# Kernel optimization log

Measured on AMD Instinct MI355X. Metric: run time of the kernel, lower is better.

The kernel has to match this reference:

```python
import jax, jax.numpy as jnp
import numpy as np

B, C, H, W = 2, 128, 64, 64


def setup_inputs() -> dict:
    key = jax.random.key(0)
    ks = jax.random.split(key, 16)
    s = 1.0 / np.sqrt(C)
    d = {
        "x": jax.random.normal(ks[0], (B, C, H, W), jnp.float32),
        "y": jax.random.normal(ks[1], (B, C, H, W), jnp.float32),
    }
    names = ["qr", "qi", "kr", "ki", "vr", "vi"]
    for i, n in enumerate(names):
        d["W" + n] = jax.random.normal(ks[2 + 2 * i], (C, C), jnp.float32) * s
        d["b" + n] = jax.random.normal(ks[3 + 2 * i], (C,), jnp.float32) * s
    return d


def _lin(t, Wt, bt):
    # t: [b, n, c]; torch Linear: t @ W^T + b
    return jnp.einsum("bnc,dc->bnd", t, Wt) + bt


def reference(x, y, Wqr, bqr, Wqi, bqi, Wkr, bkr, Wki, bki, Wvr, bvr, Wvi, bvi):
    b, c, h, w = x.shape
    xf = jnp.fft.fft2(x)  # over last two axes (h, w)
    yf = jnp.fft.fft2(y)
    # b c h w -> b (h w) c
    def flat(t):
        return t.transpose(0, 2, 3, 1).reshape(b, h * w, c)
    xr, xi = flat(xf.real), flat(xf.imag)
    yr, yi = flat(yf.real), flat(yf.imag)

    Qr = _lin(xr, Wqr, bqr) - _lin(xi, Wqi, bqi)
    Qi = _lin(xi, Wqr, bqr) + _lin(xr, Wqi, bqi)
    Kr = _lin(yr, Wkr, bkr) - _lin(yi, Wki, bki)
    Ki = _lin(yi, Wkr, bkr) + _lin(yr, Wki, bki)
    Vr = _lin(yr, Wvr, bvr) - _lin(yi, Wvi, bvi)
    Vi = _lin(yi, Wvr, bvr) + _lin(yr, Wvi, bvi)

    sr = jnp.einsum("bnc,bmc->bnm", Qr, Kr) - jnp.einsum("bnc,bmc->bnm", Qi, Ki)
    si = jnp.einsum("bnc,bmc->bnm", Qr, Ki) + jnp.einsum("bnc,bmc->bnm", Qi, Kr)
    scores = jnp.sqrt(sr * sr + si * si + 1e-8)
    attn = jax.nn.softmax(scores, axis=-1)

    out_r = jnp.einsum("bnm,bmc->bnc", attn, Vr)
    out_i = jnp.einsum("bnm,bmc->bnc", attn, Vi)
    out_c = jax.lax.complex(out_r, out_i)
    # b (h w) c -> b c h w
    out_c = out_c.reshape(b, h, w, c).transpose(0, 3, 1, 2)
    return jnp.fft.ifft2(out_c).real
```

## Files before the change

kernel.cpp:

```cpp
#include <hip/hip_runtime.h>
#include <math.h>


#define PI2 6.283185307179586f

typedef __attribute__((ext_vector_type(8))) short short8;
typedef __attribute__((ext_vector_type(4))) float f32x4;

#define MFMA16(A,B,C) __builtin_amdgcn_mfma_f32_16x16x32_bf16((A),(B),(C),0,0,0)

__device__ inline unsigned short f2bf(float x){
  union{float f; unsigned int u;} a; a.f = x;
  unsigned int r = (a.u + 0x7fffu + ((a.u>>16)&1u)) >> 16;
  return (unsigned short)r;
}
__device__ inline float bf2f(unsigned short h){
  union{unsigned int u; float f;} a; a.u = ((unsigned int)h)<<16; return a.f;
}
__device__ inline short8 neg8(short8 x){
  union{short8 v; unsigned int u[4];} a; a.v = x;
  a.u[0]^=0x80008000u; a.u[1]^=0x80008000u; a.u[2]^=0x80008000u; a.u[3]^=0x80008000u;
  return a.v;
}
__device__ inline void gload_lds16(const void* g, void* lds){
  __builtin_amdgcn_global_load_lds((const __attribute__((address_space(1))) unsigned int*)g,
                                   (__attribute__((address_space(3))) unsigned int*)lds,
                                   16, 0, 0);
}

__global__ __launch_bounds__(256) void dft2_fwd_kernel(
    const float* __restrict__ x, const float* __restrict__ y,
    float* __restrict__ xr, float* __restrict__ xi,
    float* __restrict__ yr, float* __restrict__ yi)
{
  __shared__ float Xs[4096];
  __shared__ float Tr[4096], Ti[4096];
  __shared__ float twc[64], tws[64];
  int blk = blockIdx.x;
  const float* src; float *outr, *outi;
  int plane;
  if (blk < 256) { src = x; outr = xr; outi = xi; plane = blk; }
  else           { src = y; outr = yr; outi = yi; plane = blk - 256; }
  int b = plane >> 7, c = plane & 127;
  int t = threadIdx.x;
  if (t < 64) {
    float ang = -PI2 * (float)t / 64.0f;
    twc[t] = cosf(ang); tws[t] = sinf(ang);
  }
  const float* p = src + ((size_t)plane << 12);
  for (int i = t; i < 4096; i += 256) Xs[i] = p[i];
  __syncthreads();
  for (int j = 0; j < 16; j++) {
    int o = t + 256 * j; int h = o >> 6, wp = o & 63;
    float ar = 0.f, ai = 0.f;
    for (int w = 0; w < 64; w++) {
      int k = (w * wp) & 63;
      float v = Xs[h * 64 + w];
      ar = fmaf(v, twc[k], ar);
      ai = fmaf(v, tws[k], ai);
    }
    Tr[h * 64 + wp] = ar; Ti[h * 64 + wp] = ai;
  }
  __syncthreads();
  size_t ob = ((size_t)b * 4096) * 128 + c;
  for (int j = 0; j < 16; j++) {
    int o = t + 256 * j; int hp = o >> 6, wp = o & 63;
    float ar = 0.f, ai = 0.f;
    for (int h = 0; h < 64; h++) {
      int k = (h * hp) & 63;
      float cr = twc[k], ci = tws[k];
      float tr = Tr[h * 64 + wp], ti = Ti[h * 64 + wp];
      ar += tr * cr - ti * ci;
      ai += tr * ci + ti * cr;
    }
    int n = (hp << 6) + wp;
    outr[ob + (size_t)n * 128] = ar;
    outi[ob + (size_t)n * 128] = ai;
  }
}

__global__ __launch_bounds__(256) void proj_pack_kernel(
    const float* __restrict__ xr, const float* __restrict__ xi,
    const float* __restrict__ yr, const float* __restrict__ yi,
    const float* __restrict__ Wqr, const float* __restrict__ bqr,
    const float* __restrict__ Wqi, const float* __restrict__ bqi,
    const float* __restrict__ Wkr, const float* __restrict__ bkr,
    const float* __restrict__ Wki, const float* __restrict__ bki,
    const float* __restrict__ Wvr, const float* __restrict__ bvr,
    const float* __restrict__ Wvi, const float* __restrict__ bvi,
    unsigned short* __restrict__ Qpk, unsigned short* __restrict__ Kpk,
    unsigned short* __restrict__ Vpk)
{
  __shared__ __align__(16) char smem[65536];
  float* Asr = (float*)smem;
  float* Asi = Asr + 64 * 33;
  float* Wsr = Asi + 64 * 33;
  float* Wsi = Wsr + 128 * 33;
  unsigned short* pk = (unsigned short*)smem;

  int nt = blockIdx.x, lin = blockIdx.y, b = blockIdx.z;
  const float *ar, *ai, *Wr, *Wi, *br_, *bi_;
  if (lin == 0)      { ar = xr; ai = xi; Wr = Wqr; Wi = Wqi; br_ = bqr; bi_ = bqi; }
  else if (lin == 1) { ar = yr; ai = yi; Wr = Wkr; Wi = Wki; br_ = bkr; bi_ = bki; }
  else               { ar = yr; ai = yi; Wr = Wvr; Wi = Wvi; br_ = bvr; bi_ = bvi; }
  int t = threadIdx.x; int td = t & 15, tn = t >> 4;
  int n0 = nt * 64;
  size_t abase = (size_t)b * 4096 * 128 + (size_t)n0 * 128;
  float accr[4][8] = {}, acci[4][8] = {};
  for (int kk = 0; kk < 4; kk++) {
    __syncthreads();
    for (int idx = t; idx < 64 * 32; idx += 256) {
      int r = idx >> 5, ccol = idx & 31;
      Asr[r * 33 + ccol] = ar[abase + (size_t)r * 128 + kk * 32 + ccol];
      Asi[r * 33 + ccol] = ai[abase + (size_t)r * 128 + kk * 32 + ccol];
    }
    for (int idx = t; idx < 128 * 32; idx += 256) {
      int r = idx >> 5, ccol = idx & 31;
      Wsr[r * 33 + ccol] = Wr[(size_t)r * 128 + kk * 32 + ccol];
      Wsi[r * 33 + ccol] = Wi[(size_t)r * 128 + kk * 32 + ccol];
    }
    __syncthreads();
    for (int k = 0; k < 32; k++) {
      float a_r[4], a_i[4], w_r[8], w_i[8];
      #pragma unroll
      for (int i = 0; i < 4; i++) {
        a_r[i] = Asr[(tn * 4 + i) * 33 + k];
        a_i[i] = Asi[(tn * 4 + i) * 33 + k];
      }
      #pragma unroll
      for (int jj = 0; jj < 8; jj++) {
        w_r[jj] = Wsr[(td + 16 * jj) * 33 + k];
        w_i[jj] = Wsi[(td + 16 * jj) * 33 + k];
      }
      #pragma unroll
      for (int i = 0; i < 4; i++)
        #pragma unroll
        for (int jj = 0; jj < 8; jj++) {
          accr[i][jj] += a_r[i] * w_r[jj] - a_i[i] * w_i[jj];
          acci[i][jj] += a_i[i] * w_r[jj] + a_r[i] * w_i[jj];
        }
    }
  }
  __syncthreads();
  for (int jj = 0; jj < 8; jj++) {
    int d = td + 16 * jj;
    float brd = br_[d], bid = bi_[d];
    #pragma unroll
    for (int i = 0; i < 4; i++) {
      int n = n0 + tn * 4 + i;
      float cr = accr[i][jj] + (brd - bid);
      float ci = acci[i][jj] + (brd + bid);
      if (lin <= 1) {
        unsigned short rh = f2bf(cr); unsigned short rl = f2bf(cr - bf2f(rh));
        unsigned short ih = f2bf(ci); unsigned short il = f2bf(ci - bf2f(ih));
        int s = d >> 5, j = d & 7;
        int lq = ((d & 31) >> 3) * 16 + (n & 15);
        int gi = (n >> 4) & 3;
        if (lin == 0) {
          pk[(((gi * 4 + 0) * 4 + s) * 512) + lq * 8 + j] = rh;
          pk[(((gi * 4 + 1) * 4 + s) * 512) + lq * 8 + j] = rl;
          pk[(((gi * 4 + 2) * 4 + s) * 512) + lq * 8 + j] = ih;
          pk[(((gi * 4 + 3) * 4 + s) * 512) + lq * 8 + j] = il;
        } else {
          pk[(((0 * 4 + gi) * 4 + s) * 512) + lq * 8 + j] = rh;
          pk[(((1 * 4 + gi) * 4 + s) * 512) + lq * 8 + j] = rl;
          pk[(((2 * 4 + gi) * 4 + s) * 512) + lq * 8 + j] = ih;
          pk[(((3 * 4 + gi) * 4 + s) * 512) + lq * 8 + j] = il;
        }
      } else {
        int smi = (n >> 5) & 1, jv = n & 7;
        int lv = ((n & 31) >> 3) * 16 + (d & 15);
        pk[(smi * 16 + (d >> 4)) * 512 + lv * 8 + jv] = f2bf(cr);
        pk[(smi * 16 + 8 + (d >> 4)) * 512 + lv * 8 + jv] = f2bf(ci);
      }
    }
  }
  __syncthreads();
  if (lin == 0) {
    int tq0 = nt * 4;
    #pragma unroll
    for (int ch = 0; ch < 16; ch++) {
      int idx = t + 256 * ch;
      int l = idx & 63; int rest = idx >> 6;
      int s = rest & 3, a = (rest >> 2) & 3, gi = rest >> 4;
      short8 v = *(const short8*)(pk + (size_t)idx * 8);
      size_t gaddr = ((size_t)((b * 256 + tq0 + gi) * 16 + a * 4 + s)) * 512 + (size_t)l * 8;
      *(short8*)(Qpk + gaddr) = v;
    }
  } else if (lin == 1) {
    int mt2 = n0 >> 6;
    size_t gbase = ((size_t)(b * 64 + mt2)) * 32768;
    #pragma unroll
    for (int ch = 0; ch < 16; ch++) {
      int idx = t + 256 * ch;
      short8 v = *(const short8*)(pk + (size_t)idx * 8);
      *(short8*)(Kpk + gbase + (size_t)idx * 8) = v;
    }
  } else {
    int sm0 = n0 >> 5;
    size_t gbase = ((size_t)(b * 128 + sm0)) * 8192;
    #pragma unroll
    for (int ch = 0; ch < 8; ch++) {
      int idx = t + 256 * ch;
      short8 v = *(const short8*)(pk + (size_t)idx * 8);
      *(short8*)(Vpk + gbase + (size_t)idx * 8) = v;
    }
  }
}

__global__ __launch_bounds__(512, 1) void attn_mfma_kernel(
    const short* __restrict__ Qpk, const short* __restrict__ Kpk,
    const short* __restrict__ Vpk,
    float* __restrict__ Or_, float* __restrict__ Oi_)
{
  __shared__ __align__(16) short Klds[2][32768];
  __shared__ __align__(16) short Pfrag[4 * 512];
  __shared__ float rmax[2][16][4];
  __shared__ float rsum[2][16][4];

  const int bi = blockIdx.x;
  const int xg = bi & 7;
  const int b = xg >> 2;
  const int qt = (bi >> 3) * 4 + (xg & 3);
  const int t = threadIdx.x;
  const int w = t >> 6, l = t & 63;
  const int qg = w & 1, mh = w >> 1;
  const int g = l >> 4, c = l & 15;

  const short8* Qp8 = (const short8*)Qpk;
  const int tq = qt * 2 + qg;
  short8 Qf[4][4];
  #pragma unroll
  for (int a = 0; a < 4; a++)
    #pragma unroll
    for (int s = 0; s < 4; s++)
      Qf[a][s] = Qp8[((size_t)((b * 256 + tq) * 16 + a * 4 + s)) * 64 + l];

  f32x4 O[4], M, L;
  #pragma unroll
  for (int nt = 0; nt < 4; nt++) O[nt] = (f32x4){0.f, 0.f, 0.f, 0.f};
  M = (f32x4){-3e38f, -3e38f, -3e38f, -3e38f};
  L = (f32x4){0.f, 0.f, 0.f, 0.f};

  const char* Kg = (const char*)Kpk;
  {
    const char* gsrc = Kg + ((size_t)(b * 64) << 16);
    char* lb = (char*)&Klds[0][0];
    #pragma unroll
    for (int i2 = 0; i2 < 8; i2++) {
      int ch = i2 * 8 + w;
      gload_lds16(gsrc + ch * 1024 + l * 16, lb + ch * 1024);
    }
  }
  const short8* Vp8 = (const short8*)Vpk;

  for (int mt = 0; mt < 64; mt++) {
    const int cur = mt & 1;
    __syncthreads();
    if (mt + 1 < 64) {
      const char* gsrc = Kg + ((size_t)(b * 64 + mt + 1) << 16);
      char* lb = (char*)&Klds[cur ^ 1][0];
      #pragma unroll
      for (int i2 = 0; i2 < 8; i2++) {
        int ch = i2 * 8 + w;
        gload_lds16(gsrc + ch * 1024 + l * 16, lb + ch * 1024);
      }
    }
    const short8* kb8 = (const short8*)&Klds[cur][0];
    f32x4 sr = (f32x4){0,0,0,0}, si = (f32x4){0,0,0,0};
    #pragma unroll
    for (int s = 0; s < 4; s++) {
      short8 Brh = kb8[((0 * 4 + mh) * 4 + s) * 64 + l];
      short8 Brl = kb8[((1 * 4 + mh) * 4 + s) * 64 + l];
      short8 Bih = kb8[((2 * 4 + mh) * 4 + s) * 64 + l];
      short8 Bil = kb8[((3 * 4 + mh) * 4 + s) * 64 + l];
      short8 nBih = neg8(Bih), nBil = neg8(Bil);
      sr = MFMA16(Qf[0][s], Brh, sr);
      si = MFMA16(Qf[0][s], Bih, si);
      sr = MFMA16(Qf[1][s], Brh, sr);
      si = MFMA16(Qf[1][s], Bih, si);
      sr = MFMA16(Qf[0][s], Brl, sr);
      si = MFMA16(Qf[0][s], Bil, si);
      sr = MFMA16(Qf[2][s], nBih, sr);
      si = MFMA16(Qf[2][s], Brh, si);
      sr = MFMA16(Qf[3][s], nBih, sr);
      si = MFMA16(Qf[3][s], Brh, si);
      sr = MFMA16(Qf[2][s], nBil, sr);
      si = MFMA16(Qf[2][s], Brl, si);
    }
    f32x4 s0, mx;
    #pragma unroll
    for (int r = 0; r < 4; r++) {
      s0[r] = sqrtf(sr[r] * sr[r] + si[r] * si[r] + 1e-8f);
      mx[r] = s0[r];
    }
    #pragma unroll
    for (int d = 1; d < 16; d <<= 1) {
      #pragma unroll
      for (int r = 0; r < 4; r++) mx[r] = fmaxf(mx[r], __shfl_xor(mx[r], d));
    }
    if (c < 4) rmax[qg][4 * g + c][mh] = mx[c];
    __syncthreads();
    f32x4 nm, esc, p, ps;
    #pragma unroll
    for (int r = 0; r < 4; r++) {
      float v = fmaxf(fmaxf(rmax[qg][4 * g + r][0], rmax[qg][4 * g + r][1]),
                      fmaxf(rmax[qg][4 * g + r][2], rmax[qg][4 * g + r][3]));
      nm[r] = fmaxf(M[r], v);
      esc[r] = __expf(M[r] - nm[r]);
      M[r] = nm[r];
      p[r] = __expf(s0[r] - nm[r]);
      ps[r] = p[r];
    }
    #pragma unroll
    for (int d = 1; d < 16; d <<= 1) {
      #pragma unroll
      for (int r = 0; r < 4; r++) ps[r] += __shfl_xor(ps[r], d);
    }
    if (c < 4) rsum[qg][4 * g + c][mh] = ps[c];
    {
      int ks = mh >> 1;
      int lb2 = ((mh & 1) * 2 + (c >> 3)) * 16;
      int j = c & 7;
      #pragma unroll
      for (int r = 0; r < 4; r++)
        Pfrag[(qg * 2 + ks) * 512 + (lb2 + 4 * g + r) * 8 + j] = (short)f2bf(p[r]);
    }
    __syncthreads();
    #pragma unroll
    for (int r = 0; r < 4; r++) {
      L[r] = L[r] * esc[r] + rsum[qg][4 * g + r][0] + rsum[qg][4 * g + r][1]
                           + rsum[qg][4 * g + r][2] + rsum[qg][4 * g + r][3];
      #pragma unroll
      for (int nt = 0; nt < 4; nt++) O[nt][r] *= esc[r];
    }
    #pragma unroll
    for (int ks = 0; ks < 2; ks++) {
      short8 Pa = *(const short8*)&Pfrag[(qg * 2 + ks) * 512 + l * 8];
      const size_t vb = ((size_t)((b * 128 + mt * 2 + ks) * 16 + mh * 4)) * 64 + l;
      #pragma unroll
      for (int nt = 0; nt < 4; nt++) {
        short8 Vb = Vp8[vb + (size_t)nt * 64];
        O[nt] = MFMA16(Pa, Vb, O[nt]);
      }
    }
  }
  const size_t base = (size_t)b * 4096 * 128;
  f32x4 inv;
  #pragma unroll
  for (int r = 0; r < 4; r++) inv[r] = 1.0f / L[r];
  #pragma unroll
  for (int nt = 0; nt < 4; nt++) {
    int cc = mh * 64 + nt * 16 + c;
    #pragma unroll
    for (int r = 0; r < 4; r++) {
      int row = qt * 32 + qg * 16 + 4 * g + r;
      float v = O[nt][r] * inv[r];
      if (cc < 128) Or_[base + (size_t)row * 128 + cc] = v;
      else          Oi_[base + (size_t)row * 128 + cc - 128] = v;
    }
  }
}

__global__ __launch_bounds__(256) void idft2_kernel(
    const float* __restrict__ Or_, const float* __restrict__ Oi_,
    float* __restrict__ out)
{
  __shared__ float Ar[4096], Ai[4096], Tr[4096], Ti[4096];
  __shared__ float twc[64], tws[64];
  int plane = blockIdx.x; int b = plane >> 7, c = plane & 127;
  int t = threadIdx.x;
  if (t < 64) {
    float ang = PI2 * (float)t / 64.0f;
    twc[t] = cosf(ang); tws[t] = sinf(ang);
  }
  size_t ibase = (size_t)b * 4096 * 128 + c;
  for (int i = t; i < 4096; i += 256) {
    Ar[i] = Or_[ibase + (size_t)i * 128];
    Ai[i] = Oi_[ibase + (size_t)i * 128];
  }
  __syncthreads();
  for (int j = 0; j < 16; j++) {
    int o = t + 256 * j; int hp = o >> 6, w = o & 63;
    float tr = 0.f, ti = 0.f;
    for (int wp = 0; wp < 64; wp++) {
      int k = (wp * w) & 63;
      float cr = twc[k], ci = tws[k];
      float ar = Ar[hp * 64 + wp], ai = Ai[hp * 64 + wp];
      tr += ar * cr - ai * ci;
      ti += ai * cr + ar * ci;
    }
    Tr[hp * 64 + w] = tr; Ti[hp * 64 + w] = ti;
  }
  __syncthreads();
  size_t obase = ((size_t)plane) << 12;
  for (int j = 0; j < 16; j++) {
    int o = t + 256 * j; int h = o >> 6, w = o & 63;
    float acc = 0.f;
    for (int hp = 0; hp < 64; hp++) {
      int k = (hp * h) & 63;
      acc += Tr[hp * 64 + w] * twc[k] - Ti[hp * 64 + w] * tws[k];
    }
    out[obase + o] = acc * (1.0f / 4096.0f);
  }
}

extern "C" void kernel_launch(void* const* d_in, const int* in_sizes, int n_in,
                              void* d_out, int out_size, void* d_ws, size_t ws_size,
                              hipStream_t stream) {
  const float* x   = (const float*)d_in[0];
  const float* y   = (const float*)d_in[1];
  const float* Wqr = (const float*)d_in[2];  const float* bqr = (const float*)d_in[3];
  const float* Wqi = (const float*)d_in[4];  const float* bqi = (const float*)d_in[5];
  const float* Wkr = (const float*)d_in[6];  const float* bkr = (const float*)d_in[7];
  const float* Wki = (const float*)d_in[8];  const float* bki = (const float*)d_in[9];
  const float* Wvr = (const float*)d_in[10]; const float* bvr = (const float*)d_in[11];
  const float* Wvi = (const float*)d_in[12]; const float* bvi = (const float*)d_in[13];
  char* wsb = (char*)d_ws;
  if (ws_size < ((size_t)36 << 20)) return;
  unsigned short* Qpk = (unsigned short*)(wsb);
  unsigned short* Kpk = (unsigned short*)(wsb + ((size_t)8 << 20));
  unsigned short* Vpk = (unsigned short*)(wsb + ((size_t)16 << 20));
  float* xr = (float*)(wsb + ((size_t)20 << 20));
  float* xi = (float*)(wsb + ((size_t)24 << 20));
  float* yr = (float*)(wsb + ((size_t)28 << 20));
  float* yi = (float*)(wsb + ((size_t)32 << 20));
  float* Or_ = (float*)(wsb + ((size_t)20 << 20));
  float* Oi_ = (float*)(wsb + ((size_t)24 << 20));
  float* out = (float*)d_out;

  hipLaunchKernelGGL(dft2_fwd_kernel, dim3(512), dim3(256), 0, stream,
                     x, y, xr, xi, yr, yi);
  hipLaunchKernelGGL(proj_pack_kernel, dim3(64, 3, 2), dim3(256), 0, stream,
                     xr, xi, yr, yi,
                     Wqr, bqr, Wqi, bqi, Wkr, bkr, Wki, bki, Wvr, bvr, Wvi, bvi,
                     Qpk, Kpk, Vpk);
  hipLaunchKernelGGL(attn_mfma_kernel, dim3(256), dim3(512), 0, stream,
                     (const short*)Qpk, (const short*)Kpk, (const short*)Vpk, Or_, Oi_);
  hipLaunchKernelGGL(idft2_kernel, dim3(256), dim3(256), 0, stream,
                     Or_, Oi_, out);
}
```

Baseline: 480.0 us.

## Restructure attention softmax loop to defer PV MFMA and drop a barrier

```diff
diff --git a/kernel.cpp b/kernel.cpp
--- a/kernel.cpp
+++ b/kernel.cpp
@@ -79,66 +79,65 @@
   }
 }
 
-__global__ __launch_bounds__(256) void proj_pack_kernel(
-    const float* __restrict__ xr, const float* __restrict__ xi,
-    const float* __restrict__ yr, const float* __restrict__ yi,
-    const float* __restrict__ Wqr, const float* __restrict__ bqr,
-    const float* __restrict__ Wqi, const float* __restrict__ bqi,
-    const float* __restrict__ Wkr, const float* __restrict__ bkr,
-    const float* __restrict__ Wki, const float* __restrict__ bki,
-    const float* __restrict__ Wvr, const float* __restrict__ bvr,
-    const float* __restrict__ Wvi, const float* __restrict__ bvi,
-    unsigned short* __restrict__ Qpk, unsigned short* __restrict__ Kpk,
-    unsigned short* __restrict__ Vpk)
+template<int LIN>
+__global__ __launch_bounds__(256) void proj_pack_t(
+    const float* __restrict__ ar, const float* __restrict__ ai,
+    const float* __restrict__ Wr, const float* __restrict__ Wi,
+    const float* __restrict__ br_, const float* __restrict__ bi_,
+    unsigned short* __restrict__ outp)
 {
   __shared__ __align__(16) char smem[65536];
   float* Asr = (float*)smem;
-  float* Asi = Asr + 64 * 33;
-  float* Wsr = Asi + 64 * 33;
-  float* Wsi = Wsr + 128 * 33;
+  float* Asi = Asr + 64 * 36;
+  float* Wsr = Asi + 64 * 36;
+  float* Wsi = Wsr + 128 * 36;
   unsigned short* pk = (unsigned short*)smem;
 
-  int nt = blockIdx.x, lin = blockIdx.y, b = blockIdx.z;
-  const float *ar, *ai, *Wr, *Wi, *br_, *bi_;
-  if (lin == 0)      { ar = xr; ai = xi; Wr = Wqr; Wi = Wqi; br_ = bqr; bi_ = bqi; }
-  else if (lin == 1) { ar = yr; ai = yi; Wr = Wkr; Wi = Wki; br_ = bkr; bi_ = bki; }
-  else               { ar = yr; ai = yi; Wr = Wvr; Wi = Wvi; br_ = bvr; bi_ = bvi; }
+  int nt = blockIdx.x, b = blockIdx.y;
   int t = threadIdx.x; int td = t & 15, tn = t >> 4;
   int n0 = nt * 64;
   size_t abase = (size_t)b * 4096 * 128 + (size_t)n0 * 128;
   float accr[4][8] = {}, acci[4][8] = {};
   for (int kk = 0; kk < 4; kk++) {
     __syncthreads();
-    for (int idx = t; idx < 64 * 32; idx += 256) {
-      int r = idx >> 5, ccol = idx & 31;
-      Asr[r * 33 + ccol] = ar[abase + (size_t)r * 128 + kk * 32 + ccol];
-      Asi[r * 33 + ccol] = ai[abase + (size_t)r * 128 + kk * 32 + ccol];
-    }
-    for (int idx = t; idx < 128 * 32; idx += 256) {
-      int r = idx >> 5, ccol = idx & 31;
-      Wsr[r * 33 + ccol] = Wr[(size_t)r * 128 + kk * 32 + ccol];
-      Wsi[r * 33 + ccol] = Wi[(size_t)r * 128 + kk * 32 + ccol];
+    #pragma unroll
+    for (int q2 = 0; q2 < 2; q2++) {
+      int idx = t + 256 * q2; int r = idx >> 3, c4 = (idx & 7) * 4;
+      f32x4 va = *(const f32x4*)&ar[abase + (size_t)r * 128 + kk * 32 + c4];
+      f32x4 vb = *(const f32x4*)&ai[abase + (size_t)r * 128 + kk * 32 + c4];
+      *(f32x4*)&Asr[r * 36 + c4] = va;
+      *(f32x4*)&Asi[r * 36 + c4] = vb;
+    }
+    #pragma unroll
+    for (int q2 = 0; q2 < 4; q2++) {
+      int idx = t + 256 * q2; int r = idx >> 3, c4 = (idx & 7) * 4;
+      f32x4 va = *(const f32x4*)&Wr[(size_t)r * 128 + kk * 32 + c4];
+      f32x4 vb = *(const f32x4*)&Wi[(size_t)r * 128 + kk * 32 + c4];
+      *(f32x4*)&Wsr[r * 36 + c4] = va;
+      *(f32x4*)&Wsi[r * 36 + c4] = vb;
     }
     __syncthreads();
-    for (int k = 0; k < 32; k++) {
-      float a_r[4], a_i[4], w_r[8], w_i[8];
+    for (int k4 = 0; k4 < 8; k4++) {
+      f32x4 a_r[4], a_i[4], w_r[8], w_i[8];
       #pragma unroll
       for (int i = 0; i < 4; i++) {
-        a_r[i] = Asr[(tn * 4 + i) * 33 + k];
-        a_i[i] = Asi[(tn * 4 + i) * 33 + k];
+        a_r[i] = *(const f32x4*)&Asr[(tn * 4 + i) * 36 + k4 * 4];
+        a_i[i] = *(const f32x4*)&Asi[(tn * 4 + i) * 36 + k4 * 4];
       }
       #pragma unroll
       for (int jj = 0; jj < 8; jj++) {
-        w_r[jj] = Wsr[(td + 16 * jj) * 33 + k];
-        w_i[jj] = Wsi[(td + 16 * jj) * 33 + k];
+        w_r[jj] = *(const f32x4*)&Wsr[(td + 16 * jj) * 36 + k4 * 4];
+        w_i[jj] = *(const f32x4*)&Wsi[(td + 16 * jj) * 36 + k4 * 4];
       }
       #pragma unroll
       for (int i = 0; i < 4; i++)
         #pragma unroll
-        for (int jj = 0; jj < 8; jj++) {
-          accr[i][jj] += a_r[i] * w_r[jj] - a_i[i] * w_i[jj];
-          acci[i][jj] += a_i[i] * w_r[jj] + a_r[i] * w_i[jj];
-        }
+        for (int jj = 0; jj < 8; jj++)
+          #pragma unroll
+          for (int e = 0; e < 4; e++) {
+            accr[i][jj] += a_r[i][e] * w_r[jj][e] - a_i[i][e] * w_i[jj][e];
+            acci[i][jj] += a_i[i][e] * w_r[jj][e] + a_r[i][e] * w_i[jj][e];
+          }
     }
   }
   __syncthreads();
@@ -150,13 +149,13 @@
       int n = n0 + tn * 4 + i;
       float cr = accr[i][jj] + (brd - bid);
       float ci = acci[i][jj] + (brd + bid);
-      if (lin <= 1) {
+      if constexpr (LIN <= 1) {
         unsigned short rh = f2bf(cr); unsigned short rl = f2bf(cr - bf2f(rh));
         unsigned short ih = f2bf(ci); unsigned short il = f2bf(ci - bf2f(ih));
         int s = d >> 5, j = d & 7;
         int lq = ((d & 31) >> 3) * 16 + (n & 15);
         int gi = (n >> 4) & 3;
-        if (lin == 0) {
+        if constexpr (LIN == 0) {
           pk[(((gi * 4 + 0) * 4 + s) * 512) + lq * 8 + j] = rh;
           pk[(((gi * 4 + 1) * 4 + s) * 512) + lq * 8 + j] = rl;
           pk[(((gi * 4 + 2) * 4 + s) * 512) + lq * 8 + j] = ih;
@@ -176,7 +175,7 @@
     }
   }
   __syncthreads();
-  if (lin == 0) {
+  if constexpr (LIN == 0) {
     int tq0 = nt * 4;
     #pragma unroll
     for (int ch = 0; ch < 16; ch++) {
@@ -185,25 +184,23 @@
       int s = rest & 3, a = (rest >> 2) & 3, gi = rest >> 4;
       short8 v = *(const short8*)(pk + (size_t)idx * 8);
       size_t gaddr = ((size_t)((b * 256 + tq0 + gi) * 16 + a * 4 + s)) * 512 + (size_t)l * 8;
-      *(short8*)(Qpk + gaddr) = v;
-    }
-  } else if (lin == 1) {
-    int mt2 = n0 >> 6;
-    size_t gbase = ((size_t)(b * 64 + mt2)) * 32768;
+      *(short8*)(outp + gaddr) = v;
+    }
+  } else if constexpr (LIN == 1) {
+    size_t gbase = ((size_t)(b * 64 + (n0 >> 6))) * 32768;
     #pragma unroll
     for (int ch = 0; ch < 16; ch++) {
       int idx = t + 256 * ch;
       short8 v = *(const short8*)(pk + (size_t)idx * 8);
-      *(short8*)(Kpk + gbase + (size_t)idx * 8) = v;
+      *(short8*)(outp + gbase + (size_t)idx * 8) = v;
     }
   } else {
-    int sm0 = n0 >> 5;
-    size_t gbase = ((size_t)(b * 128 + sm0)) * 8192;
+    size_t gbase = ((size_t)(b * 128 + (n0 >> 5))) * 8192;
     #pragma unroll
     for (int ch = 0; ch < 8; ch++) {
       int idx = t + 256 * ch;
       short8 v = *(const short8*)(pk + (size_t)idx * 8);
-      *(short8*)(Vpk + gbase + (size_t)idx * 8) = v;
+      *(short8*)(outp + gbase + (size_t)idx * 8) = v;
     }
   }
 }
@@ -214,9 +211,9 @@
     float* __restrict__ Or_, float* __restrict__ Oi_)
 {
   __shared__ __align__(16) short Klds[2][32768];
-  __shared__ __align__(16) short Pfrag[4 * 512];
-  __shared__ float rmax[2][16][4];
-  __shared__ float rsum[2][16][4];
+  __shared__ __align__(16) short Pfrag[2 * 16 * 72];
+  __shared__ __align__(16) float rmax[2][16][4];
+  __shared__ __align__(16) float escs[2][16];
 
   const int bi = blockIdx.x;
   const int xg = bi & 7;
@@ -224,7 +221,7 @@
   const int qt = (bi >> 3) * 4 + (xg & 3);
   const int t = threadIdx.x;
   const int w = t >> 6, l = t & 63;
-  const int qg = w & 1, mh = w >> 1;
+  const int qg = w & 1, ms = w >> 1;
   const int g = l >> 4, c = l & 15;
 
   const short8* Qp8 = (const short8*)Qpk;
@@ -236,11 +233,14 @@
     for (int s = 0; s < 4; s++)
       Qf[a][s] = Qp8[((size_t)((b * 256 + tq) * 16 + a * 4 + s)) * 64 + l];
 
-  f32x4 O[4], M, L;
+  f32x4 O[4], Oe;
   #pragma unroll
   for (int nt = 0; nt < 4; nt++) O[nt] = (f32x4){0.f, 0.f, 0.f, 0.f};
-  M = (f32x4){-3e38f, -3e38f, -3e38f, -3e38f};
-  L = (f32x4){0.f, 0.f, 0.f, 0.f};
+  Oe = (f32x4){0.f, 0.f, 0.f, 0.f};
+  float Mq = -3e38f;
+  short8 Vreg[2][4];
+  const short b1 = (short)0x3F80;
+  const short8 ones = {b1, b1, b1, b1, b1, b1, b1, b1};
 
   const char* Kg = (const char*)Kpk;
   {
@@ -248,11 +248,12 @@
     char* lb = (char*)&Klds[0][0];
     #pragma unroll
     for (int i2 = 0; i2 < 8; i2++) {
-      int ch = i2 * 8 + w;
+      int ch = w + 8 * i2;
       gload_lds16(gsrc + ch * 1024 + l * 16, lb + ch * 1024);
     }
   }
   const short8* Vp8 = (const short8*)Vpk;
+  f32x4 s0;
 
   for (int mt = 0; mt < 64; mt++) {
     const int cur = mt & 1;
@@ -262,96 +263,105 @@
       char* lb = (char*)&Klds[cur ^ 1][0];
       #pragma unroll
       for (int i2 = 0; i2 < 8; i2++) {
-        int ch = i2 * 8 + w;
+        int ch = w + 8 * i2;
         gload_lds16(gsrc + ch * 1024 + l * 16, lb + ch * 1024);
       }
     }
+    if (mt > 0) {
+      f32x4 ev = *(const f32x4*)&escs[qg][4 * g];
+      #pragma unroll
+      for (int r = 0; r < 4; r++) {
+        #pragma unroll
+        for (int nt = 0; nt < 4; nt++) O[nt][r] *= ev[r];
+        Oe[r] *= ev[r];
+      }
+      #pragma unroll
+      for (int ks = 0; ks < 2; ks++) {
+        short8 Pa = *(const short8*)&Pfrag[(qg * 16 + c) * 72 + 32 * ks + 8 * g];
+        #pragma unroll
+        for (int nt = 0; nt < 4; nt++)
+          O[nt] = MFMA16(Pa, Vreg[ks][nt], O[nt]);
+        Oe = MFMA16(Pa, ones, Oe);
+      }
+    }
     const short8* kb8 = (const short8*)&Klds[cur][0];
-    f32x4 sr = (f32x4){0,0,0,0}, si = (f32x4){0,0,0,0};
+    f32x4 sr = (f32x4){0, 0, 0, 0}, si = (f32x4){0, 0, 0, 0};
     #pragma unroll
     for (int s = 0; s < 4; s++) {
-      short8 Brh = kb8[((0 * 4 + mh) * 4 + s) * 64 + l];
-      short8 Brl = kb8[((1 * 4 + mh) * 4 + s) * 64 + l];
-      short8 Bih = kb8[((2 * 4 + mh) * 4 + s) * 64 + l];
-      short8 Bil = kb8[((3 * 4 + mh) * 4 + s) * 64 + l];
-      short8 nBih = neg8(Bih), nBil = neg8(Bil);
-      sr = MFMA16(Qf[0][s], Brh, sr);
-      si = MFMA16(Qf[0][s], Bih, si);
-      sr = MFMA16(Qf[1][s], Brh, sr);
-      si = MFMA16(Qf[1][s], Bih, si);
-      sr = MFMA16(Qf[0][s], Brl, sr);
-      si = MFMA16(Qf[0][s], Bil, si);
-      sr = MFMA16(Qf[2][s], nBih, sr);
-      si = MFMA16(Qf[2][s], Brh, si);
-      sr = MFMA16(Qf[3][s], nBih, sr);
-      si = MFMA16(Qf[3][s], Brh, si);
-      sr = MFMA16(Qf[2][s], nBil, sr);
-      si = MFMA16(Qf[2][s], Brl, si);
-    }
-    f32x4 s0, mx;
+      short8 Arh = kb8[((0 * 4 + ms) * 4 + s) * 64 + l];
+      short8 Arl = kb8[((1 * 4 + ms) * 4 + s) * 64 + l];
+      short8 Aih = kb8[((2 * 4 + ms) * 4 + s) * 64 + l];
+      short8 Ail = kb8[((3 * 4 + ms) * 4 + s) * 64 + l];
+      short8 nqh = neg8(Qf[2][s]);
+      short8 nql = neg8(Qf[3][s]);
+      sr = MFMA16(Arh, Qf[0][s], sr);
+      si = MFMA16(Arh, Qf[2][s], si);
+      sr = MFMA16(Arh, Qf[1][s], sr);
+      si = MFMA16(Arh, Qf[3][s], si);
+      sr = MFMA16(Arl, Qf[0][s], sr);
+      si = MFMA16(Arl, Qf[2][s], si);
+      sr = MFMA16(Aih, nqh, sr);
+      si = MFMA16(Aih, Qf[0][s], si);
+      sr = MFMA16(Aih, nql, sr);
+      si = MFMA16(Aih, Qf[1][s], si);
+      sr = MFMA16(Ail, nqh, sr);
+      si = MFMA16(Ail, Qf[0][s], si);
+    }
+    float mloc;
+    #pragma unroll
+    for (int r = 0; r < 4; r++)
+      s0[r] = sqrtf(sr[r] * sr[r] + si[r] * si[r] + 1e-8f);
+    mloc = fmaxf(fmaxf(s0[0], s0[1]), fmaxf(s0[2], s0[3]));
+    mloc = fmaxf(mloc, __shfl_xor(mloc, 16));
+    mloc = fmaxf(mloc, __shfl_xor(mloc, 32));
+    if (l < 16) rmax[qg][l][ms] = mloc;
+    __syncthreads();
+    {
+      f32x4 rm4 = *(const f32x4*)&rmax[qg][c][0];
+      float nmq = fmaxf(fmaxf(rm4[0], rm4[1]), fmaxf(rm4[2], rm4[3]));
+      nmq = fmaxf(Mq, nmq);
+      float escq = __expf(Mq - nmq);
+      Mq = nmq;
+      if (ms == 0 && l < 16) escs[qg][l] = escq;
+      #pragma unroll
+      for (int ks = 0; ks < 2; ks++)
+        #pragma unroll
+        for (int nt = 0; nt < 4; nt++)
+          Vreg[ks][nt] = Vp8[((size_t)((b * 128 + mt * 2 + ks) * 16 + ms * 4 + nt)) * 64 + l];
+      f32x4 p;
+      #pragma unroll
+      for (int r = 0; r < 4; r++) p[r] = __expf(s0[r] - nmq);
+      unsigned int w01 = (unsigned int)f2bf(p[0]) | ((unsigned int)f2bf(p[1]) << 16);
+      unsigned int w23 = (unsigned int)f2bf(p[2]) | ((unsigned int)f2bf(p[3]) << 16);
+      unsigned int* pw = (unsigned int*)&Pfrag[(qg * 16 + c) * 72 + 16 * ms + 4 * g];
+      pw[0] = w01; pw[1] = w23;
+    }
+  }
+  __syncthreads();
+  {
+    f32x4 ev = *(const f32x4*)&escs[qg][4 * g];
     #pragma unroll
     for (int r = 0; r < 4; r++) {
-      s0[r] = sqrtf(sr[r] * sr[r] + si[r] * si[r] + 1e-8f);
-      mx[r] = s0[r];
-    }
-    #pragma unroll
-    for (int d = 1; d < 16; d <<= 1) {
-      #pragma unroll
-      for (int r = 0; r < 4; r++) mx[r] = fmaxf(mx[r], __shfl_xor(mx[r], d));
-    }
-    if (c < 4) rmax[qg][4 * g + c][mh] = mx[c];
-    __syncthreads();
-    f32x4 nm, esc, p, ps;
-    #pragma unroll
-    for (int r = 0; r < 4; r++) {
-      float v = fmaxf(fmaxf(rmax[qg][4 * g + r][0], rmax[qg][4 * g + r][1]),
-                      fmaxf(rmax[qg][4 * g + r][2], rmax[qg][4 * g + r][3]));
-      nm[r] = fmaxf(M[r], v);
-      esc[r] = __expf(M[r] - nm[r]);
-      M[r] = nm[r];
-      p[r] = __expf(s0[r] - nm[r]);
-      ps[r] = p[r];
-    }
-    #pragma unroll
-    for (int d = 1; d < 16; d <<= 1) {
-      #pragma unroll
-      for (int r = 0; r < 4; r++) ps[r] += __shfl_xor(ps[r], d);
-    }
-    if (c < 4) rsum[qg][4 * g + c][mh] = ps[c];
-    {
-      int ks = mh >> 1;
-      int lb2 = ((mh & 1) * 2 + (c >> 3)) * 16;
-      int j = c & 7;
-      #pragma unroll
-      for (int r = 0; r < 4; r++)
-        Pfrag[(qg * 2 + ks) * 512 + (lb2 + 4 * g + r) * 8 + j] = (short)f2bf(p[r]);
-    }
-    __syncthreads();
-    #pragma unroll
-    for (int r = 0; r < 4; r++) {
-      L[r] = L[r] * esc[r] + rsum[qg][4 * g + r][0] + rsum[qg][4 * g + r][1]
-                           + rsum[qg][4 * g + r][2] + rsum[qg][4 * g + r][3];
-      #pragma unroll
-      for (int nt = 0; nt < 4; nt++) O[nt][r] *= esc[r];
+      #pragma unroll
+      for (int nt = 0; nt < 4; nt++) O[nt][r] *= ev[r];
+      Oe[r] *= ev[r];
     }
     #pragma unroll
     for (int ks = 0; ks < 2; ks++) {
-      short8 Pa = *(const short8*)&Pfrag[(qg * 2 + ks) * 512 + l * 8];
-      const size_t vb = ((size_t)((b * 128 + mt * 2 + ks) * 16 + mh * 4)) * 64 + l;
-      #pragma unroll
-      for (int nt = 0; nt < 4; nt++) {
-        short8 Vb = Vp8[vb + (size_t)nt * 64];
-        O[nt] = MFMA16(Pa, Vb, O[nt]);
-      }
+      short8 Pa = *(const short8*)&Pfrag[(qg * 16 + c) * 72 + 32 * ks + 8 * g];
+      #pragma unroll
+      for (int nt = 0; nt < 4; nt++)
+        O[nt] = MFMA16(Pa, Vreg[ks][nt], O[nt]);
+      Oe = MFMA16(Pa, ones, Oe);
     }
   }
   const size_t base = (size_t)b * 4096 * 128;
   f32x4 inv;
   #pragma unroll
-  for (int r = 0; r < 4; r++) inv[r] = 1.0f / L[r];
+  for (int r = 0; r < 4; r++) inv[r] = 1.0f / Oe[r];
   #pragma unroll
   for (int nt = 0; nt < 4; nt++) {
-    int cc = mh * 64 + nt * 16 + c;
+    int cc = ms * 64 + nt * 16 + c;
     #pragma unroll
     for (int r = 0; r < 4; r++) {
       int row = qt * 32 + qg * 16 + 4 * g + r;
@@ -431,10 +441,12 @@
 
   hipLaunchKernelGGL(dft2_fwd_kernel, dim3(512), dim3(256), 0, stream,
                      x, y, xr, xi, yr, yi);
-  hipLaunchKernelGGL(proj_pack_kernel, dim3(64, 3, 2), dim3(256), 0, stream,
-                     xr, xi, yr, yi,
-                     Wqr, bqr, Wqi, bqi, Wkr, bkr, Wki, bki, Wvr, bvr, Wvi, bvi,
-                     Qpk, Kpk, Vpk);
+  hipLaunchKernelGGL(proj_pack_t<0>, dim3(64, 2), dim3(256), 0, stream,
+                     xr, xi, Wqr, Wqi, bqr, bqi, Qpk);
+  hipLaunchKernelGGL(proj_pack_t<1>, dim3(64, 2), dim3(256), 0, stream,
+                     yr, yi, Wkr, Wki, bkr, bki, Kpk);
+  hipLaunchKernelGGL(proj_pack_t<2>, dim3(64, 2), dim3(256), 0, stream,
+                     yr, yi, Wvr, Wvi, bvr, bvi, Vpk);
   hipLaunchKernelGGL(attn_mfma_kernel, dim3(256), dim3(512), 0, stream,
                      (const short*)Qpk, (const short*)Kpk, (const short*)Vpk, Or_, Oi_);
   hipLaunchKernelGGL(idft2_kernel, dim3(256), dim3(256), 0, stream,
```

New measurement: 462.4 us. 3.7% less time.
